# Kernel optimization log

Hardware: AMD Instinct MI355X
Metric: run time of the kernel (lower is better)

Reference implementation:

```python
import jax, jax.numpy as jnp
import numpy as np

SCORE_THRESH = 0.25
NMS_THRESH = 0.45
DET_PER_IMG = 300
PRE_NMS_TOPK = 2048  # fixed-size candidate set replacing dynamic torch.where


def setup_inputs() -> dict:
    key = jax.random.key(0)
    k1, k2, k3, k4 = jax.random.split(key, 4)
    B, N, C5 = 16, 25200, 85  # YOLOv5 @640: 3*(80^2+40^2+20^2)=25200 anchors, 80 classes + 5
    head_outputs = jax.random.normal(k1, (B, N, C5), jnp.float32)
    grid = jax.random.uniform(k2, (N, 2), jnp.float32) * 80.0          # cell coords
    anchor_grid = jax.random.uniform(k3, (N, 2), jnp.float32) * 60.0 + 4.0  # anchor w/h in px
    stride = 8.0 * (1.0 + jax.random.uniform(k4, (N, 1), jnp.float32))      # per-anchor stride
    return {"head_outputs": head_outputs, "grid": grid,
            "anchor_grid": anchor_grid, "stride": stride}


def _pairwise_iou(b):
    # b: [K,4] xyxy -> [K,K] IoU
    area = (b[:, 2] - b[:, 0]) * (b[:, 3] - b[:, 1])
    lt = jnp.maximum(b[:, None, :2], b[None, :, :2])
    rb = jnp.minimum(b[:, None, 2:], b[None, :, 2:])
    wh = jnp.clip(rb - lt, 0.0)
    inter = wh[..., 0] * wh[..., 1]
    return inter / (area[:, None] + area[None, :] - inter + 1e-7)


def _nms_keep(boxes, valid, thr):
    # boxes sorted by descending score; greedy suppression via scan
    K = boxes.shape[0]
    iou = _pairwise_iou(boxes)
    def body(keep, i):
        row = jnp.where(keep[i], iou[i] <= thr, True)  # i suppresses overlapping j only if kept
        row = row.at[i].set(keep[i])                   # never self-suppress
        return keep & row, None
    keep, _ = jax.lax.scan(body, valid, jnp.arange(K))
    return keep


def _postprocess_single(head, grid, anchor_grid, stride):
    p = jax.nn.sigmoid(head)                     # [N, 85]
    scores = p[:, 5:] * p[:, 4:5]                # [N, C] class * objectness
    N, C = scores.shape
    # BoxCoder.decode_single (cxcywh -> xyxy)
    xy = (p[:, :2] * 2.0 - 0.5 + grid) * stride  # [N,2]
    wh = (p[:, 2:4] * 2.0) ** 2 * anchor_grid    # [N,2]
    boxes = jnp.concatenate([xy - wh * 0.5, xy + wh * 0.5], axis=1)  # [N,4]

    # torch.where(scores > thresh) -> fixed-size top-k over flattened (anchor, class)
    flat = jnp.where(scores > SCORE_THRESH, scores, -1.0).reshape(-1)
    top_s, top_i = jax.lax.top_k(flat, PRE_NMS_TOPK)
    a_idx = top_i // C
    labels = (top_i % C).astype(jnp.int32)
    cand = boxes[a_idx]                          # [K,4]
    valid = top_s > 0.0

    # batched_nms: per-class coordinate offset so classes never overlap
    offset = (jnp.max(cand) + 1.0) * labels.astype(cand.dtype)[:, None]
    keep = _nms_keep(cand + offset, valid, NMS_THRESH)

    kept_s = jnp.where(keep, top_s, -1.0)
    fs, fi = jax.lax.top_k(kept_s, DET_PER_IMG)  # keep[:detections_per_img]
    ok = fs > 0.0
    fb = jnp.where(ok[:, None], cand[fi], 0.0)
    fl = jnp.where(ok, labels[fi], -1)
    return fb, fs, fl


def reference(head_outputs, grid, anchor_grid, stride):
    boxes, scores, labels = jax.vmap(
        lambda h: _postprocess_single(h, grid, anchor_grid, stride))(head_outputs)
    # padded analogue of List[Dict]: boxes [B,300,4], scores [B,300], labels [B,300]
    return boxes, scores, labels
```

## Files before the change

kernel.cpp:

```cpp
#include <hip/hip_runtime.h>
#include <hip/hip_bf16.h>

#define B    16
#define NA   25200
#define NCH  85
#define NCLS 80
#define K    2048
#define CAP  4096
#define ACAP 4096
#define DET  300
#define TILE 64
#define NTILES 394
#define PBLK 64
#define LBUF 2304
#define SBASE  0x3FD0000000000000ULL
#define SSHIFT 42

typedef unsigned long long u64;
typedef unsigned int u32;
typedef unsigned short u16;
typedef unsigned char u8;

__device__ __forceinline__ double dsig(float x) { return 1.0 / (1.0 + exp(-(double)x)); }
__device__ __forceinline__ float  fsig(float x) { return 1.0f / (1.0f + __expf(-x)); }

__global__ void __launch_bounds__(256) k_hist(const float* __restrict__ head,
                                              u32* __restrict__ phist, u16* __restrict__ smax16) {
    __shared__ float rows[TILE * NCH];
    __shared__ int h[2048];
    __shared__ float smaxT[TILE][4];
    int tid = threadIdx.x;
    int hblk = gridDim.x;
    for (int i = tid; i < 2048; i += 256) h[i] = 0;
    int img = blockIdx.y;
    const float* ibase = head + (size_t)img * NA * NCH;

    float4 pf[6];
    int tile = blockIdx.x;
    {
        int a0 = tile * TILE;
        int na = NA - a0; if (na > TILE) na = TILE;
        int nf4 = (na * NCH) >> 2;
        const float4* src = (const float4*)(ibase + (size_t)a0 * NCH);
        #pragma unroll
        for (int u = 0; u < 6; ++u) { int i = tid + u * 256; pf[u] = (i < nf4) ? src[i] : make_float4(0.f,0.f,0.f,0.f); }
    }
    for (; tile < NTILES; tile += hblk) {
        int a0 = tile * TILE;
        int na = NA - a0; if (na > TILE) na = TILE;
        int nf4 = (na * NCH) >> 2;
        __syncthreads();
        #pragma unroll
        for (int u = 0; u < 6; ++u) { int i = tid + u * 256; if (i < nf4) ((float4*)rows)[i] = pf[u]; }
        __syncthreads();
        int nt = tile + hblk;
        if (nt < NTILES) {
            int a0n = nt * TILE;
            int nan_ = NA - a0n; if (nan_ > TILE) nan_ = TILE;
            int nf4n = (nan_ * NCH) >> 2;
            const float4* srcn = (const float4*)(ibase + (size_t)a0n * NCH);
            #pragma unroll
            for (int u = 0; u < 6; ++u) { int i = tid + u * 256; pf[u] = (i < nf4n) ? srcn[i] : make_float4(0.f,0.f,0.f,0.f); }
        }
        for (int t = tid; t < 4 * na; t += 256) {
            int a = t >> 2, q = t & 3;
            float fo = fsig(rows[a * NCH + 4]);
            float lm = 0.0f;
            if (fo > 0.25f) {
                float qq = 0.24975f / fo;
                float cth = __logf(qq) - __logf(1.0f - qq);
                int c0 = q * 20;
                for (int c = c0; c < c0 + 20; ++c) {
                    float cl = rows[a * NCH + 5 + c];
                    if (cl > cth) {
                        float sc = fo * fsig(cl);
                        lm = fmaxf(lm, sc);
                        if (sc > 0.25f) {
                            u64 bits = (u64)__double_as_longlong((double)sc);
                            int bb = (int)((bits - SBASE) >> SSHIFT);
                            if (bb > 2047) bb = 2047;
                            atomicAdd(&h[bb], 1);
                        }
                    }
                }
            }
            smaxT[a][q] = lm;
        }
        __syncthreads();
        for (int t = tid; t < na; t += 256) {
            float m = fmaxf(fmaxf(smaxT[t][0], smaxT[t][1]), fmaxf(smaxT[t][2], smaxT[t][3]));
            u32 mb = __float_as_uint(m);
            smax16[(size_t)img * NA + a0 + t] = (u16)((mb + 0xFFFFu) >> 16);
        }
    }
    __syncthreads();
    u32* dst = phist + ((size_t)img * hblk + blockIdx.x) * 2048;
    for (int i = tid; i < 2048; i += 256) dst[i] = (u32)h[i];
}

__global__ void __launch_bounds__(256) k_redsum(const u32* __restrict__ phist,
                                                int* __restrict__ hist, int hblk,
                                                u32* __restrict__ cnt, u32* __restrict__ cntA) {
    int img = blockIdx.x;
    int bin = blockIdx.y * 256 + threadIdx.x;
    if (blockIdx.y == 0 && threadIdx.x == 0) cnt[img] = 0;
    if (blockIdx.y == 0 && threadIdx.x == 1) cntA[img] = 0;
    const u32* base = phist + (size_t)img * hblk * 2048 + bin;
    u32 s = 0;
    int p = 0;
    for (; p + 4 <= hblk; p += 4) {
        u32 a0 = base[(size_t)(p + 0) * 2048];
        u32 a1 = base[(size_t)(p + 1) * 2048];
        u32 a2 = base[(size_t)(p + 2) * 2048];
        u32 a3 = base[(size_t)(p + 3) * 2048];
        s += a0 + a1 + a2 + a3;
    }
    for (; p < hblk; ++p) s += base[(size_t)p * 2048];
    hist[img * 2048 + bin] = (int)s;
}

__global__ void __launch_bounds__(1024) k_cut(const int* __restrict__ hist, u64* __restrict__ cut) {
    int lane = threadIdx.x & 63;
    int img  = threadIdx.x >> 6;
    const int* h = hist + img * 2048;
    int v[32];
    #pragma unroll
    for (int ch = 0; ch < 32; ++ch) v[ch] = h[2047 - ch * 64 - lane];
    int cum = 0; u64 cb = 0;
    #pragma unroll
    for (int ch = 0; ch < 32; ++ch) {
        int pfx = v[ch];
        for (int d = 1; d < 64; d <<= 1) { int o = __shfl_up(pfx, d, 64); if (lane >= d) pfx += o; }
        u64 ball = __ballot(cum + pfx >= K);
        if (ball) {
            int fl = __ffsll((long long)ball) - 1;
            int bin = 2047 - ch * 64 - fl;
            cb = (bin >= 1) ? (SBASE + ((u64)(bin - 1) << SSHIFT)) : 0ULL;
            break;
        }
        cum += __shfl(pfx, 63, 64);
    }
    if (lane == 0) cut[img] = cb;
}

__global__ void __launch_bounds__(256) k_screen(const u16* __restrict__ smax16, const u64* __restrict__ cut,
                                                u32* __restrict__ cntA, int* __restrict__ alist) {
    __shared__ int lcnt, lbase, buf[256];
    int img = blockIdx.y;
    int a = blockIdx.x * 256 + threadIdx.x;
    if (threadIdx.x == 0) lcnt = 0;
    __syncthreads();
    u64 cutb = cut[img];
    float cutf = cutb ? (float)__longlong_as_double((long long)cutb) : 0.25f;
    float pre = fmaxf(0.2489f, cutf * 0.999f);
    if (a < NA) {
        float fup = __uint_as_float(((u32)smax16[(size_t)img * NA + a]) << 16);
        if (fup >= pre) buf[atomicAdd(&lcnt, 1)] = a;
    }
    __syncthreads();
    if (threadIdx.x == 0 && lcnt) lbase = atomicAdd(&cntA[img], (u32)lcnt);
    __syncthreads();
    for (int i = threadIdx.x; i < lcnt; i += 256) {
        int pos = lbase + i;
        if (pos < ACAP) alist[img * ACAP + pos] = buf[i];
    }
}

__global__ void __launch_bounds__(256) k_pairs(const float* __restrict__ head, const u64* __restrict__ cut,
                                               const float* __restrict__ grid, const float* __restrict__ ag,
                                               const float* __restrict__ stv,
                                               const u32* __restrict__ cntA, const int* __restrict__ alist,
                                               u32* __restrict__ cnt, u64* __restrict__ sb, u32* __restrict__ si,
                                               double* __restrict__ boxg) {
    __shared__ u64 lsb[LBUF];
    __shared__ u32 lsi[LBUF];
    __shared__ u32 lcnt, lbase;
    int img = blockIdx.y;
    int tid = threadIdx.x;
    u64 cutb = cut[img];
    float cutf = cutb ? (float)__longlong_as_double((long long)cutb) : 0.25f;
    float pre = fmaxf(0.2489f, cutf * 0.999f);
    int nsur = (int)cntA[img]; if (nsur > ACAP) nsur = ACAP;
    int npairs = nsur * NCLS;
    u64* sbi = sb + (size_t)img * CAP;
    u32* sii = si + (size_t)img * CAP;
    const float* ibase = head + (size_t)img * NA * NCH;
    if (tid == 0) lcnt = 0;
    __syncthreads();

    int base = blockIdx.x * 256;
    int ntrip = (npairs > base) ? (npairs - base + PBLK * 256 - 1) / (PBLK * 256) : 0;
    for (int t = 0; t <= ntrip; ++t) {
        if (t < ntrip) {
            int p = base + tid + t * PBLK * 256;
            if (p < npairs) {
                int ai = (int)((u32)p / NCLS);
                int c  = p - ai * NCLS;
                int a  = alist[img * ACAP + ai];
                const float* row = ibase + (size_t)a * NCH;
                float o = row[4], cl = row[5 + c];
                float s32 = fsig(o) * fsig(cl);
                if (s32 >= pre) {
                    double sc = dsig(o) * dsig(cl);
                    if (sc > 0.25) {
                        u64 bits = (u64)__double_as_longlong(sc);
                        if (bits >= cutb) {
                            u32 pos = atomicAdd(&lcnt, 1u);
                            if (pos < LBUF) { lsb[pos] = bits; lsi[pos] = (u32)(a * NCLS + c); }
                        }
                    }
                }
            }
        }
        __syncthreads();
        bool last = (t == ntrip);
        if ((!last && lcnt >= 2048) || (last && lcnt > 0)) {
            u32 n = lcnt; if (n > LBUF) n = LBUF;
            if (tid == 0) lbase = atomicAdd(&cnt[img], n);
            __syncthreads();
            for (u32 i = tid; i < n; i += 256) {
                u32 pos = lbase + i;
                if (pos < CAP) {
                    u32 idx = lsi[i];
                    sbi[pos] = lsb[i]; sii[pos] = idx;
                    int a = (int)(idx / NCLS);
                    const float* row = ibase + (size_t)a * NCH;
                    double p0 = dsig(row[0]), p1 = dsig(row[1]), p2 = dsig(row[2]), p3 = dsig(row[3]);
                    double st = (double)stv[a];
                    double xc = (p0 * 2.0 - 0.5 + (double)grid[a * 2 + 0]) * st;
                    double yc = (p1 * 2.0 - 0.5 + (double)grid[a * 2 + 1]) * st;
                    double w = p2 * 2.0; w = (w * w) * (double)ag[a * 2 + 0];
                    double h = p3 * 2.0; h = (h * h) * (double)ag[a * 2 + 1];
                    double* bg = boxg + ((size_t)img * CAP + pos) * 4;
                    bg[0] = xc - w * 0.5; bg[1] = yc - h * 0.5;
                    bg[2] = xc + w * 0.5; bg[3] = yc + h * 0.5;
                }
            }
            __syncthreads();
            if (tid == 0) lcnt = 0;
            __syncthreads();
        }
    }
}

__global__ void __launch_bounds__(1024) k_sortp(const u32* __restrict__ cntArr,
                                                u64* __restrict__ sb, u32* __restrict__ si,
                                                u16* __restrict__ permg, u8* __restrict__ keptg) {
    __shared__ u64 TA[4096];
    __shared__ u32 TI[4096];
    __shared__ u16 TP[4096];
    __shared__ u32 h2[2048];
    __shared__ u32 cntb[2048];
    __shared__ u32 segtot[32];
    int img = blockIdx.x;
    int tid = threadIdx.x;
    int lane = tid & 63, wv = tid >> 6;
    u32* tmp = TI;

    u64* A = sb + (size_t)img * CAP;
    u32* I = si + (size_t)img * CAP;
    int cnt = (int)cntArr[img]; if (cnt > CAP) cnt = CAP;

    keptg[(size_t)img * 2048 + tid] = 1;
    keptg[(size_t)img * 2048 + 1024 + tid] = 1;

    for (int b = tid; b < 2048; b += 1024) h2[b] = 0;
    __syncthreads();
    for (int e = tid; e < cnt; e += 1024) {
        u64 bits = A[e];
        int b = (int)((bits - SBASE) >> SSHIFT);
        b = b < 0 ? 0 : (b > 2047 ? 2047 : b);
        atomicAdd(&h2[b], 1u);
    }
    __syncthreads();
    for (int s = wv; s < 32; s += 16) {
        int r = s * 64 + lane;
        u32 v = h2[2047 - r];
        cntb[2047 - r] = v;
        u32 p = v;
        for (int d = 1; d < 64; d <<= 1) { u32 o = __shfl_up(p, d, 64); if (lane >= d) p += o; }
        if (lane == 63) segtot[s] = p;
        tmp[r] = p - v;
    }
    __syncthreads();
    if (tid < 32) {
        u32 v = segtot[tid], p = v;
        for (int d = 1; d < 32; d <<= 1) { u32 o = __shfl_up(p, d, 64); if (lane >= d) p += o; }
        segtot[tid] = p - v;
    }
    __syncthreads();
    for (int s = wv; s < 32; s += 16) {
        int r = s * 64 + lane;
        h2[2047 - r] = tmp[r] + segtot[s];
    }
    __syncthreads();
    for (int e = tid; e < 4096; e += 1024) if (e >= cnt) { TA[e] = 0ULL; TI[e] = 0xFFFFFFFFu; TP[e] = 0; }
    __syncthreads();
    for (int e = tid; e < cnt; e += 1024) {
        u64 bits = A[e]; u32 idx = I[e];
        int b = (int)((bits - SBASE) >> SSHIFT);
        b = b < 0 ? 0 : (b > 2047 ? 2047 : b);
        u32 slot = atomicAdd(&h2[b], 1u);
        if (slot < 4096u) { TA[slot] = bits; TI[slot] = idx; TP[slot] = (u16)e; }
    }
    __syncthreads();
    u64 rb[4]; u32 ri[4]; int rp[4]; u16 rq[4];
    #pragma unroll
    for (int s4 = 0; s4 < 4; ++s4) {
        int p = tid + s4 * 1024;
        rp[s4] = -1;
        if (p < cnt) {
            u64 kb = TA[p]; u32 ki = TI[p]; u16 kq = TP[p];
            int b = (int)((kb - SBASE) >> SSHIFT);
            b = b < 0 ? 0 : (b > 2047 ? 2047 : b);
            int en = (int)h2[b];
            int st = en - (int)cntb[b];
            int r = st;
            for (int j = st; j < en; ++j) {
                u64 b2 = TA[j]; u32 i2 = TI[j];
                if (b2 > kb || (b2 == kb && i2 < ki)) ++r;
            }
            rb[s4] = kb; ri[s4] = ki; rq[s4] = kq; rp[s4] = r;
        }
    }
    __syncthreads();
    #pragma unroll
    for (int s4 = 0; s4 < 4; ++s4)
        if (rp[s4] >= 0 && rp[s4] < 4096) { TA[rp[s4]] = rb[s4]; TI[rp[s4]] = ri[s4]; TP[rp[s4]] = rq[s4]; }
    __syncthreads();
    A[tid] = TA[tid];               I[tid] = TI[tid];
    A[1024 + tid] = TA[1024 + tid]; I[1024 + tid] = TI[1024 + tid];
    permg[(size_t)img * 2048 + tid]        = TP[tid];
    permg[(size_t)img * 2048 + 1024 + tid] = TP[1024 + tid];
}

#define NMS_FRONT_HALF                                                          \
    u64 sv[2]; u32 fidx[2];                                                     \
    sv[0] = A[tid];        fidx[0] = I[tid];                                    \
    sv[1] = A[1024 + tid]; fidx[1] = I[1024 + tid];                             \
    if (tid < NCLS) clscnt[tid] = 0;                                            \
    for (int i = tid; i < 32 * NCLS; i += 1024) ((u32*)chunkcnt)[i] = 0;        \
    double bx[2][4];                                                            \
    int lab[2];                                                                 \
    bool val[2];                                                                \
    double lmax = -1e300, lmin = 1e300;                                         \
    __syncthreads();                                                            \
    _Pragma("unroll")                                                           \
    for (int q = 0; q < 2; ++q) {                                               \
        int slot = q * 1024 + tid;                                              \
        val[q] = (sv[q] != 0ULL);                                               \
        bx[q][0] = bx[q][1] = bx[q][2] = bx[q][3] = 0.0;                        \
        lab[q] = 0;                                                             \
        if (val[q]) {                                                           \
            lab[q] = (int)(fidx[q] % NCLS);                                     \
            int p = (int)permg[(size_t)img * 2048 + slot];                      \
            const double* bg = boxg + ((size_t)img * CAP + p) * 4;              \
            bx[q][0] = bg[0]; bx[q][1] = bg[1];                                 \
            bx[q][2] = bg[2]; bx[q][3] = bg[3];                                 \
            lmax = fmax(lmax, fmax(fmax(bx[q][0], bx[q][1]), fmax(bx[q][2], bx[q][3]))); \
            lmin = fmin(lmin, fmin(fmin(bx[q][0], bx[q][1]), fmin(bx[q][2], bx[q][3]))); \
            atomicAdd(&clscnt[lab[q]], 1);                                      \
            atomicAdd(&chunkcnt[slot >> 6][lab[q]], 1u);                        \
        }                                                                       \
        labs[slot] = val[q] ? (u16)lab[q] : (u16)0xFFFF;                        \
    }                                                                           \
    for (int d = 1; d < 64; d <<= 1) {                                          \
        lmax = fmax(lmax, __shfl_xor(lmax, d, 64));                             \
        lmin = fmin(lmin, __shfl_xor(lmin, d, 64));                             \
    }                                                                           \
    if (lane == 0) { red[wv] = lmax; red2[wv] = lmin; }                         \
    __syncthreads();                                                            \
    if (tid == 0) {                                                             \
        double m = red[0], mn = red2[0];                                        \
        for (int w2 = 1; w2 < 16; ++w2) { m = fmax(m, red[w2]); mn = fmin(mn, red2[w2]); } \
        s_offb = m + 1.0;                                                       \
        s_viol2 = (m + 2.0 + mn < 0.0) ? 1 : 0;                                 \
    }                                                                           \
    __syncthreads();                                                            \
    double offb = s_offb;                                                       \
    double oB[2][4], aR[2];                                                     \
    _Pragma("unroll")                                                           \
    for (int q = 0; q < 2; ++q) {                                               \
        double off = offb * (double)lab[q];                                     \
        oB[q][0] = bx[q][0] + off; oB[q][1] = bx[q][1] + off;                   \
        oB[q][2] = bx[q][2] + off; oB[q][3] = bx[q][3] + off;                   \
        aR[q] = (oB[q][2] - oB[q][0]) * (oB[q][3] - oB[q][1]);                  \
        int slot = q * 1024 + tid;                                              \
        obm[0][slot] = oB[q][0]; obm[1][slot] = oB[q][1];                       \
        obm[2][slot] = oB[q][2]; obm[3][slot] = oB[q][3];                       \
    }                                                                           \
    __syncthreads();                                                            \
    if (tid < 64) {                                                             \
        int c0 = clscnt[lane];                                                  \
        int c1 = (lane < NCLS - 64) ? clscnt[64 + lane] : 0;                    \
        int p0 = c0;                                                            \
        for (int d = 1; d < 64; d <<= 1) { int o = __shfl_up(p0, d, 64); if (lane >= d) p0 += o; } \
        int tot0 = __shfl(p0, 63, 64);                                          \
        int p1 = c1;                                                            \
        for (int d = 1; d < 64; d <<= 1) { int o = __shfl_up(p1, d, 64); if (lane >= d) p1 += o; } \
        clsbase[lane] = p0 - c0;                                                \
        if (lane < NCLS - 64) clsbase[64 + lane] = tot0 + p1 - c1;              \
        if (lane == 63) clsbase[NCLS] = tot0 + __shfl(p1, NCLS - 64 - 1, 64);   \
    }                                                                           \
    __syncthreads();                                                            \
    if (tid < NCLS) {                                                           \
        int running = clsbase[tid];                                             \
        for (int ch = 0; ch < 32; ++ch) {                                       \
            u32 t = chunkcnt[ch][tid];                                          \
            chunkcnt[ch][tid] = (u32)running;                                   \
            running += (int)t;                                                  \
        }                                                                       \
    }                                                                           \
    __syncthreads();                                                            \
    _Pragma("unroll")                                                           \
    for (int q = 0; q < 2; ++q) {                                               \
        int cl = val[q] ? lab[q] : -1;                                          \
        int rank = 0;                                                           \
        for (int d = 1; d < 64; ++d) {                                          \
            int oc = __shfl_up(cl, d, 64);                                      \
            if (lane >= d && oc == cl) ++rank;                                  \
        }                                                                       \
        if (val[q]) {                                                           \
            int slot = q * 1024 + tid;                                          \
            seg[chunkcnt[slot >> 6][cl] + rank] = (u16)slot;                    \
        }                                                                       \
    }                                                                           \
    __syncthreads();

__global__ void __launch_bounds__(1024) k_greedy(const u64* __restrict__ sb, const u32* __restrict__ si,
        const u16* __restrict__ permg, const double* __restrict__ boxg, u8* __restrict__ keptg) {
    __shared__ double obm[4][K];
    __shared__ u16 labs[K];
    __shared__ u16 seg[K];
    __shared__ u32 chunkcnt[32][NCLS];
    __shared__ int clsbase[NCLS + 1];
    __shared__ int clscnt[NCLS];
    __shared__ double red[16], red2[16];
    __shared__ double s_offb;
    __shared__ int s_viol2;
    __shared__ u64 amw[16][32];

    int img = blockIdx.x;
    int tid = threadIdx.x;
    int lane = tid & 63, wv = tid >> 6;
    const u64* A = sb + (size_t)img * CAP;
    const u32* I = si + (size_t)img * CAP;

    NMS_FRONT_HALF

    int c = blockIdx.y * 16 + wv;
    int cbase = clsbase[c];
    int m = clsbase[c + 1] - cbase;
    u8* kp = keptg + (size_t)img * 2048;
    if (m > 1) {
        if (m <= 64) {
            int s_l = (lane < m) ? (int)seg[cbase + lane] : -1;
            double e0 = 0, e1 = 0, e2 = 0, e3 = 0, ea = 0;
            if (s_l >= 0) {
                e0 = obm[0][s_l]; e1 = obm[1][s_l];
                e2 = obm[2][s_l]; e3 = obm[3][s_l];
                ea = (e2 - e0) * (e3 - e1);
            }
            u64 ovl = 0ULL;
            for (int k = 0; k < m; ++k) {
                double k0 = __shfl(e0, k, 64), k1 = __shfl(e1, k, 64);
                double k2 = __shfl(e2, k, 64), k3 = __shfl(e3, k, 64);
                double ka = __shfl(ea, k, 64);
                double ww = fmax(fmin(k2, e2) - fmax(k0, e0), 0.0);
                double hh = fmax(fmin(k3, e3) - fmax(k1, e1), 0.0);
                double inter = ww * hh;
                bool o = (lane > k) && (lane < m) &&
                         (inter > 0.45 * (ka + ea - inter + 1e-7));
                ovl |= o ? (1ULL << k) : 0ULL;
            }
            u64 live = (m >= 64) ? ~0ULL : ((1ULL << m) - 1ULL);
            for (int k = 0; k < m; ++k) {
                u64 kill = __ballot((ovl >> k) & 1ULL);
                if ((live >> k) & 1ULL) live &= ~kill;
            }
            if (s_l >= 0 && !((live >> lane) & 1ULL)) kp[s_l] = 0;
        } else {
            u64* AM = amw[wv];
            if (lane < 32) {
                int lo = lane * 64;
                AM[lane] = (m >= lo + 64) ? ~0ULL : (m > lo ? ((1ULL << (m - lo)) - 1ULL) : 0ULL);
            }
            for (int k = 0; k < m; ++k) {
                if (!((AM[k >> 6] >> (k & 63)) & 1ULL)) continue;
                int sk = (int)seg[cbase + k];
                double k0 = obm[0][sk], k1 = obm[1][sk];
                double k2 = obm[2][sk], k3 = obm[3][sk];
                double ka = (k2 - k0) * (k3 - k1);
                for (int j = k + 1 + lane; j < m; j += 64) {
                    if (!((AM[j >> 6] >> (j & 63)) & 1ULL)) continue;
                    int t = (int)seg[cbase + j];
                    double b0 = obm[0][t], b1 = obm[1][t];
                    double b2 = obm[2][t], b3 = obm[3][t];
                    double ww = fmax(fmin(k2, b2) - fmax(k0, b0), 0.0);
                    double hh = fmax(fmin(k3, b3) - fmax(k1, b1), 0.0);
                    double inter = ww * hh;
                    double aj = (b2 - b0) * (b3 - b1);
                    if (inter > 0.45 * (ka + aj - inter + 1e-7))
                        atomicAnd(&AM[j >> 6], ~(1ULL << (j & 63)));
                }
            }
            for (int j = lane; j < m; j += 64)
                if (!((AM[j >> 6] >> (j & 63)) & 1ULL)) kp[(int)seg[cbase + j]] = 0;
        }
    }
}

__global__ void __launch_bounds__(1024) k_fin(const u64* __restrict__ sb, const u32* __restrict__ si,
        const u16* __restrict__ permg, const double* __restrict__ boxg,
        const u8* __restrict__ keptg, float* __restrict__ out) {
    __shared__ double obm[4][K];
    __shared__ u16 labs[K];
    __shared__ u16 seg[K];
    __shared__ u32 chunkcnt[32][NCLS];
    __shared__ int clsbase[NCLS + 1];
    __shared__ int clscnt[NCLS];
    __shared__ double red[16], red2[16];
    __shared__ double s_offb;
    __shared__ int s_viol2;
    __shared__ u64 mask[32], imask[32];
    __shared__ int wpfx[33];
    __shared__ int viol;

    int img = blockIdx.x;
    int tid = threadIdx.x;
    int lane = tid & 63, wv = tid >> 6;
    const u64* A = sb + (size_t)img * CAP;
    const u32* I = si + (size_t)img * CAP;

    NMS_FRONT_HALF

    const u8* kp = keptg + (size_t)img * 2048;
    {
        bool k0 = val[0] && (kp[tid] != 0);
        bool k1 = val[1] && (kp[1024 + tid] != 0);
        u64 m0 = __ballot(k0), m1 = __ballot(k1);
        u64 v0 = __ballot(val[0]), v1 = __ballot(val[1]);
        if (lane == 0) { mask[wv] = m0; mask[16 + wv] = m1; imask[wv] = v0; imask[16 + wv] = v1; }
    }
    if (tid == 0) viol = s_viol2;
    __syncthreads();

    #pragma unroll
    for (int q = 0; q < 2; ++q) {
        int s = q * 1024 + tid;
        if ((mask[s >> 6] >> (s & 63)) & 1ULL) {
            int myc = (int)labs[s];
            float c0 = (float)obm[0][s], c1 = (float)obm[1][s];
            float c2v = (float)obm[2][s], c3 = (float)obm[3][s];
            float ca = (c2v - c0) * (c3 - c1);
            #pragma unroll
            for (int dd = 0; dd < 2; ++dd) {
                int cc = myc + (dd ? 1 : -1);
                if (cc < 0 || cc >= NCLS) continue;
                int je = clsbase[cc + 1];
                for (int j = clsbase[cc]; j < je; ++j) {
                    int t = (int)seg[j];
                    if (t > s) {
                        float b0 = (float)obm[0][t], b1 = (float)obm[1][t];
                        float b2 = (float)obm[2][t], b3 = (float)obm[3][t];
                        float ww = fmaxf(fminf(c2v, b2) - fmaxf(c0, b0), 0.f);
                        float hh = fmaxf(fminf(c3, b3) - fmaxf(c1, b1), 0.f);
                        float inter = ww * hh;
                        float aj = (b2 - b0) * (b3 - b1);
                        if (inter > 0.4485f * (ca + aj - inter + 1e-7f)) viol = 1;
                    }
                }
            }
        }
    }
    __syncthreads();

    if (viol) {
        if (tid < 32) mask[tid] = imask[tid];
        bool alive[2]; alive[0] = val[0]; alive[1] = val[1];
        __syncthreads();
        int i = -1, kc = 0;
        while (true) {
            int start = i + 1;
            if (start >= K) break;
            int w = start >> 6;
            u64 m = mask[w] & (~0ULL << (start & 63));
            while (m == 0ULL) { if (++w >= 32) break; m = mask[w]; }
            if (w >= 32) break;
            i = (w << 6) + __ffsll((long long)m) - 1;
            ++kc;
            if (kc >= DET) break;
            double bi0 = obm[0][i], bi1 = obm[1][i];
            double bi2 = obm[2][i], bi3 = obm[3][i];
            double ai = (bi2 - bi0) * (bi3 - bi1);
            #pragma unroll
            for (int q = 0; q < 2; ++q) {
                int slot = q * 1024 + tid;
                double w_ = fmax(fmin(bi2, oB[q][2]) - fmax(bi0, oB[q][0]), 0.0);
                double h_ = fmax(fmin(bi3, oB[q][3]) - fmax(bi1, oB[q][1]), 0.0);
                double inter = w_ * h_;
                bool sup = inter > 0.45 * (ai + aR[q] - inter + 1e-7);
                if (alive[q] && slot > i && sup) {
                    alive[q] = false;
                    atomicAnd(&mask[slot >> 6], ~(1ULL << (slot & 63)));
                }
            }
            __syncthreads();
        }
        __syncthreads();
    }

    if (tid == 0) {
        int s = 0;
        for (int w2 = 0; w2 < 32; ++w2) { wpfx[w2] = s; s += __popcll(mask[w2]); }
        wpfx[32] = s;
    }
    __syncthreads();
    int total = wpfx[32]; if (total > DET) total = DET;

    float* bo  = out + (size_t)img * DET * 4;
    float* so_ = out + (size_t)B * DET * 4 + (size_t)img * DET;
    float* lo  = out + (size_t)B * DET * 5 + (size_t)img * DET;
    #pragma unroll
    for (int q = 0; q < 2; ++q) {
        int slot = q * 1024 + tid;
        int w = slot >> 6, bpos = slot & 63;
        if ((mask[w] >> bpos) & 1ULL) {
            int r = wpfx[w] + __popcll(mask[w] & ((1ULL << bpos) - 1ULL));
            if (r < DET) {
                bo[r * 4 + 0] = (float)bx[q][0]; bo[r * 4 + 1] = (float)bx[q][1];
                bo[r * 4 + 2] = (float)bx[q][2]; bo[r * 4 + 3] = (float)bx[q][3];
                so_[r] = (float)__longlong_as_double((long long)sv[q]);
                lo[r] = (float)lab[q];
            }
        }
    }
    if (tid >= total && tid < DET) {
        bo[tid * 4 + 0] = 0.f; bo[tid * 4 + 1] = 0.f;
        bo[tid * 4 + 2] = 0.f; bo[tid * 4 + 3] = 0.f;
        so_[tid] = -1.0f; lo[tid] = -1.0f;
    }
}

extern "C" void kernel_launch(void* const* d_in, const int* in_sizes, int n_in,
                              void* d_out, int out_size, void* d_ws, size_t ws_size,
                              hipStream_t stream) {
    const float* head = (const float*)d_in[0];
    const float* grid = (const float*)d_in[1];
    const float* ag   = (const float*)d_in[2];
    const float* stv  = (const float*)d_in[3];
    float* out = (float*)d_out;
    char* ws = (char*)d_ws;

    u64* sb     = (u64*)(ws + 0);
    u32* si     = (u32*)(ws + 524288);
    int* alist  = (int*)(ws + 786432);
    u16* permg  = (u16*)(ws + 786432);
    u8*  keptg  = (u8*)(ws + 851968);
    u32* cnt    = (u32*)(ws + 1048576);
    u32* cntA   = (u32*)(ws + 1048640);
    u64* cut    = (u64*)(ws + 1048704);
    u16* smax16 = (u16*)(ws + 1048832);
    int* hist   = (int*)(ws + 1855232);
    u32* phist  = (u32*)(ws + 1986304);
    double* boxg = (double*)(ws + 1986304);

    int hblk = 16;
    if (ws_size >= (size_t)1986304 + (size_t)B * 128 * 2048 * 4) hblk = 128;
    else if (ws_size >= (size_t)1986304 + (size_t)B * 64 * 2048 * 4) hblk = 64;

    k_hist   <<<dim3(hblk, B), 256, 0, stream>>>(head, phist, smax16);
    k_redsum <<<dim3(B, 8), 256, 0, stream>>>(phist, hist, hblk, cnt, cntA);
    k_cut    <<<1, 1024, 0, stream>>>(hist, cut);
    k_screen <<<dim3((NA + 255) / 256, B), 256, 0, stream>>>(smax16, cut, cntA, alist);
    k_pairs  <<<dim3(PBLK, B), 256, 0, stream>>>(head, cut, grid, ag, stv, cntA, alist, cnt, sb, si, boxg);
    k_sortp  <<<B, 1024, 0, stream>>>(cnt, sb, si, permg, keptg);
    k_greedy <<<dim3(B, 5), 1024, 0, stream>>>(sb, si, permg, boxg, keptg);
    k_fin    <<<B, 1024, 0, stream>>>(sb, si, permg, boxg, keptg, out);
}
```

Before: 186.4 us.

## Move cross-class violation check into greedy kernel and fast-path final compaction

The check for IoU overlap between adjacent classes moves from k_fin into k_greedy. Each wave checks its own class segment and records a per-image violation flag in global memory, which k_sortp resets. k_fin reads that flag and, when no violation occurred, skips the NMS front half (sort and box staging into shared memory) and compacts kept detections straight from global buffers. This removes redundant front-half work in the final kernel, at the cost of more work in k_greedy and an extra global flag with atomics.

```diff
diff --git a/kernel.cpp b/kernel.cpp
--- a/kernel.cpp
+++ b/kernel.cpp
@@ -245,7 +245,8 @@
 
 __global__ void __launch_bounds__(1024) k_sortp(const u32* __restrict__ cntArr,
                                                 u64* __restrict__ sb, u32* __restrict__ si,
-                                                u16* __restrict__ permg, u8* __restrict__ keptg) {
+                                                u16* __restrict__ permg, u8* __restrict__ keptg,
+                                                int* __restrict__ violg) {
     __shared__ u64 TA[4096];
     __shared__ u32 TI[4096];
     __shared__ u16 TP[4096];
@@ -263,6 +264,7 @@
 
     keptg[(size_t)img * 2048 + tid] = 1;
     keptg[(size_t)img * 2048 + 1024 + tid] = 1;
+    if (tid == 0) violg[img] = 0;
 
     for (int b = tid; b < 2048; b += 1024) h2[b] = 0;
     __syncthreads();
@@ -428,7 +430,8 @@
     __syncthreads();
 
 __global__ void __launch_bounds__(1024) k_greedy(const u64* __restrict__ sb, const u32* __restrict__ si,
-        const u16* __restrict__ permg, const double* __restrict__ boxg, u8* __restrict__ keptg) {
+        const u16* __restrict__ permg, const double* __restrict__ boxg,
+        u8* __restrict__ keptg, int* __restrict__ violg) {
     __shared__ double obm[4][K];
     __shared__ u16 labs[K];
     __shared__ u16 seg[K];
@@ -447,6 +450,8 @@
     const u32* I = si + (size_t)img * CAP;
 
     NMS_FRONT_HALF
+
+    if (tid == 0 && s_viol2) atomicOr(&violg[img], 1);
 
     int c = blockIdx.y * 16 + wv;
     int cbase = clsbase[c];
@@ -508,54 +513,18 @@
                 if (!((AM[j >> 6] >> (j & 63)) & 1ULL)) kp[(int)seg[cbase + j]] = 0;
         }
     }
-}
-
-__global__ void __launch_bounds__(1024) k_fin(const u64* __restrict__ sb, const u32* __restrict__ si,
-        const u16* __restrict__ permg, const double* __restrict__ boxg,
-        const u8* __restrict__ keptg, float* __restrict__ out) {
-    __shared__ double obm[4][K];
-    __shared__ u16 labs[K];
-    __shared__ u16 seg[K];
-    __shared__ u32 chunkcnt[32][NCLS];
-    __shared__ int clsbase[NCLS + 1];
-    __shared__ int clscnt[NCLS];
-    __shared__ double red[16], red2[16];
-    __shared__ double s_offb;
-    __shared__ int s_viol2;
-    __shared__ u64 mask[32], imask[32];
-    __shared__ int wpfx[33];
-    __shared__ int viol;
-
-    int img = blockIdx.x;
-    int tid = threadIdx.x;
-    int lane = tid & 63, wv = tid >> 6;
-    const u64* A = sb + (size_t)img * CAP;
-    const u32* I = si + (size_t)img * CAP;
-
-    NMS_FRONT_HALF
-
-    const u8* kp = keptg + (size_t)img * 2048;
+
     {
-        bool k0 = val[0] && (kp[tid] != 0);
-        bool k1 = val[1] && (kp[1024 + tid] != 0);
-        u64 m0 = __ballot(k0), m1 = __ballot(k1);
-        u64 v0 = __ballot(val[0]), v1 = __ballot(val[1]);
-        if (lane == 0) { mask[wv] = m0; mask[16 + wv] = m1; imask[wv] = v0; imask[16 + wv] = v1; }
-    }
-    if (tid == 0) viol = s_viol2;
-    __syncthreads();
-
-    #pragma unroll
-    for (int q = 0; q < 2; ++q) {
-        int s = q * 1024 + tid;
-        if ((mask[s >> 6] >> (s & 63)) & 1ULL) {
-            int myc = (int)labs[s];
+        int cend = cbase + m;
+        bool bad = false;
+        for (int ii = cbase + lane; ii < cend; ii += 64) {
+            int s = (int)seg[ii];
             float c0 = (float)obm[0][s], c1 = (float)obm[1][s];
             float c2v = (float)obm[2][s], c3 = (float)obm[3][s];
             float ca = (c2v - c0) * (c3 - c1);
             #pragma unroll
             for (int dd = 0; dd < 2; ++dd) {
-                int cc = myc + (dd ? 1 : -1);
+                int cc = c + (dd ? 1 : -1);
                 if (cc < 0 || cc >= NCLS) continue;
                 int je = clsbase[cc + 1];
                 for (int j = clsbase[cc]; j < je; ++j) {
@@ -567,48 +536,119 @@
                         float hh = fmaxf(fminf(c3, b3) - fmaxf(c1, b1), 0.f);
                         float inter = ww * hh;
                         float aj = (b2 - b0) * (b3 - b1);
-                        if (inter > 0.4485f * (ca + aj - inter + 1e-7f)) viol = 1;
+                        if (inter > 0.4485f * (ca + aj - inter + 1e-7f)) bad = true;
                     }
                 }
             }
         }
-    }
-    __syncthreads();
-
-    if (viol) {
-        if (tid < 32) mask[tid] = imask[tid];
-        bool alive[2]; alive[0] = val[0]; alive[1] = val[1];
+        if (__ballot(bad)) { if (lane == 0) atomicOr(&violg[img], 1); }
+    }
+}
+
+__global__ void __launch_bounds__(1024) k_fin(const u64* __restrict__ sb, const u32* __restrict__ si,
+        const u16* __restrict__ permg, const double* __restrict__ boxg,
+        const u8* __restrict__ keptg, const int* __restrict__ violg, float* __restrict__ out) {
+    __shared__ double obm[4][K];
+    __shared__ u16 labs[K];
+    __shared__ u16 seg[K];
+    __shared__ u32 chunkcnt[32][NCLS];
+    __shared__ int clsbase[NCLS + 1];
+    __shared__ int clscnt[NCLS];
+    __shared__ double red[16], red2[16];
+    __shared__ double s_offb;
+    __shared__ int s_viol2;
+    __shared__ u64 mask[32];
+    __shared__ int wpfx[33];
+
+    int img = blockIdx.x;
+    int tid = threadIdx.x;
+    int lane = tid & 63, wv = tid >> 6;
+    const u64* A = sb + (size_t)img * CAP;
+    const u32* I = si + (size_t)img * CAP;
+
+    float* bo  = out + (size_t)img * DET * 4;
+    float* so_ = out + (size_t)B * DET * 4 + (size_t)img * DET;
+    float* lo  = out + (size_t)B * DET * 5 + (size_t)img * DET;
+
+    if (violg[img] == 0) {
+        u64 s0 = A[tid], s1 = A[1024 + tid];
+        u32 f0 = I[tid], f1 = I[1024 + tid];
+        const u8* kp = keptg + (size_t)img * 2048;
+        bool k0 = (s0 != 0ULL) && (kp[tid] != 0);
+        bool k1 = (s1 != 0ULL) && (kp[1024 + tid] != 0);
+        u64 m0 = __ballot(k0), m1 = __ballot(k1);
+        if (lane == 0) { mask[wv] = m0; mask[16 + wv] = m1; }
         __syncthreads();
-        int i = -1, kc = 0;
-        while (true) {
-            int start = i + 1;
-            if (start >= K) break;
-            int w = start >> 6;
-            u64 m = mask[w] & (~0ULL << (start & 63));
-            while (m == 0ULL) { if (++w >= 32) break; m = mask[w]; }
-            if (w >= 32) break;
-            i = (w << 6) + __ffsll((long long)m) - 1;
-            ++kc;
-            if (kc >= DET) break;
-            double bi0 = obm[0][i], bi1 = obm[1][i];
-            double bi2 = obm[2][i], bi3 = obm[3][i];
-            double ai = (bi2 - bi0) * (bi3 - bi1);
-            #pragma unroll
-            for (int q = 0; q < 2; ++q) {
-                int slot = q * 1024 + tid;
-                double w_ = fmax(fmin(bi2, oB[q][2]) - fmax(bi0, oB[q][0]), 0.0);
-                double h_ = fmax(fmin(bi3, oB[q][3]) - fmax(bi1, oB[q][1]), 0.0);
-                double inter = w_ * h_;
-                bool sup = inter > 0.45 * (ai + aR[q] - inter + 1e-7);
-                if (alive[q] && slot > i && sup) {
-                    alive[q] = false;
-                    atomicAnd(&mask[slot >> 6], ~(1ULL << (slot & 63)));
+        if (tid == 0) {
+            int s = 0;
+            for (int w2 = 0; w2 < 32; ++w2) { wpfx[w2] = s; s += __popcll(mask[w2]); }
+            wpfx[32] = s;
+        }
+        __syncthreads();
+        int total = wpfx[32]; if (total > DET) total = DET;
+        #pragma unroll
+        for (int q = 0; q < 2; ++q) {
+            int slot = q * 1024 + tid;
+            int w = slot >> 6, bpos = slot & 63;
+            if ((mask[w] >> bpos) & 1ULL) {
+                int r = wpfx[w] + __popcll(mask[w] & ((1ULL << bpos) - 1ULL));
+                if (r < DET) {
+                    int p = (int)permg[(size_t)img * 2048 + slot];
+                    const double* bg = boxg + ((size_t)img * CAP + p) * 4;
+                    bo[r * 4 + 0] = (float)bg[0]; bo[r * 4 + 1] = (float)bg[1];
+                    bo[r * 4 + 2] = (float)bg[2]; bo[r * 4 + 3] = (float)bg[3];
+                    u64 sv_ = q ? s1 : s0;
+                    u32 fi_ = q ? f1 : f0;
+                    so_[r] = (float)__longlong_as_double((long long)sv_);
+                    lo[r] = (float)(fi_ % NCLS);
                 }
             }
-            __syncthreads();
+        }
+        if (tid >= total && tid < DET) {
+            bo[tid * 4 + 0] = 0.f; bo[tid * 4 + 1] = 0.f;
+            bo[tid * 4 + 2] = 0.f; bo[tid * 4 + 3] = 0.f;
+            so_[tid] = -1.0f; lo[tid] = -1.0f;
+        }
+        return;
+    }
+
+    NMS_FRONT_HALF
+
+    {
+        u64 v0 = __ballot(val[0]), v1 = __ballot(val[1]);
+        if (lane == 0) { mask[wv] = v0; mask[16 + wv] = v1; }
+    }
+    bool alive[2]; alive[0] = val[0]; alive[1] = val[1];
+    __syncthreads();
+    int i = -1, kc = 0;
+    while (true) {
+        int start = i + 1;
+        if (start >= K) break;
+        int w = start >> 6;
+        u64 m = mask[w] & (~0ULL << (start & 63));
+        while (m == 0ULL) { if (++w >= 32) break; m = mask[w]; }
+        if (w >= 32) break;
+        i = (w << 6) + __ffsll((long long)m) - 1;
+        ++kc;
+        if (kc >= DET) break;
+        double bi0 = obm[0][i], bi1 = obm[1][i];
+        double bi2 = obm[2][i], bi3 = obm[3][i];
+        double ai = (bi2 - bi0) * (bi3 - bi1);
+        #pragma unroll
+        for (int q = 0; q < 2; ++q) {
+            int slot = q * 1024 + tid;
+            double w_ = fmax(fmin(bi2, oB[q][2]) - fmax(bi0, oB[q][0]), 0.0);
+            double h_ = fmax(fmin(bi3, oB[q][3]) - fmax(bi1, oB[q][1]), 0.0);
+            double inter = w_ * h_;
+            bool sup = inter > 0.45 * (ai + aR[q] - inter + 1e-7);
+            if (alive[q] && slot > i && sup) {
+                alive[q] = false;
+                atomicAnd(&mask[slot >> 6], ~(1ULL << (slot & 63)));
+            }
         }
         __syncthreads();
     }
+    __syncthreads();
 
     if (tid == 0) {
         int s = 0;
@@ -618,9 +658,6 @@
     __syncthreads();
     int total = wpfx[32]; if (total > DET) total = DET;
 
-    float* bo  = out + (size_t)img * DET * 4;
-    float* so_ = out + (size_t)B * DET * 4 + (size_t)img * DET;
-    float* lo  = out + (size_t)B * DET * 5 + (size_t)img * DET;
     #pragma unroll
     for (int q = 0; q < 2; ++q) {
         int slot = q * 1024 + tid;
@@ -657,6 +694,7 @@
     int* alist  = (int*)(ws + 786432);
     u16* permg  = (u16*)(ws + 786432);
     u8*  keptg  = (u8*)(ws + 851968);
+    int* violg  = (int*)(ws + 884736);
     u32* cnt    = (u32*)(ws + 1048576);
     u32* cntA   = (u32*)(ws + 1048640);
     u64* cut    = (u64*)(ws + 1048704);
@@ -674,7 +712,7 @@
     k_cut    <<<1, 1024, 0, stream>>>(hist, cut);
     k_screen <<<dim3((NA + 255) / 256, B), 256, 0, stream>>>(smax16, cut, cntA, alist);
     k_pairs  <<<dim3(PBLK, B), 256, 0, stream>>>(head, cut, grid, ag, stv, cntA, alist, cnt, sb, si, boxg);
-    k_sortp  <<<B, 1024, 0, stream>>>(cnt, sb, si, permg, keptg);
-    k_greedy <<<dim3(B, 5), 1024, 0, stream>>>(sb, si, permg, boxg, keptg);
-    k_fin    <<<B, 1024, 0, stream>>>(sb, si, permg, boxg, keptg, out);
-}
+    k_sortp  <<<B, 1024, 0, stream>>>(cnt, sb, si, permg, keptg, violg);
+    k_greedy <<<dim3(B, 5), 1024, 0, stream>>>(sb, si, permg, boxg, keptg, violg);
+    k_fin    <<<B, 1024, 0, stream>>>(sb, si, permg, boxg, keptg, violg, out);
+}
```

Result: faster. 154.9 us, median of 2 (-16.9%).
